# Optimization experiments

Hardware: AMD Instinct MI355X
Metric: run time of the kernel (lower is better)

Reference implementation:

```python
import jax, jax.numpy as jnp
import numpy as np
import math

HIDDEN = 1024
HEADS = 16
HEAD_DIM = HIDDEN // HEADS
B, S = 4, 2048


def setup_inputs() -> dict:
    key = jax.random.key(0)
    ks = jax.random.split(key, 10)
    scale = 1.0 / math.sqrt(HIDDEN)
    inp = {
        "x": jax.random.normal(ks[0], (B, S, HIDDEN), dtype=jnp.float32),
        "attention_mask": jnp.ones((B, 1, 1, S), dtype=jnp.int32),
        "Wq": jax.random.normal(ks[1], (HIDDEN, HIDDEN), dtype=jnp.float32) * scale,
        "bq": jnp.zeros((HIDDEN,), dtype=jnp.float32),
        "Wk": jax.random.normal(ks[2], (HIDDEN, HIDDEN), dtype=jnp.float32) * scale,
        "bk": jnp.zeros((HIDDEN,), dtype=jnp.float32),
        "Wv": jax.random.normal(ks[3], (HIDDEN, HIDDEN), dtype=jnp.float32) * scale,
        "bv": jnp.zeros((HIDDEN,), dtype=jnp.float32),
        "Wo": jax.random.normal(ks[4], (HIDDEN, HIDDEN), dtype=jnp.float32) * scale,
        "bo": jnp.zeros((HIDDEN,), dtype=jnp.float32),
    }
    return inp


def reference(x, attention_mask, Wq, bq, Wk, bk, Wv, bv, Wo, bo):
    b, s, d = x.shape
    # nn.Linear: x @ W.T + b
    q = (x @ Wq.T + bq).reshape(b, s, HEADS, HEAD_DIM).transpose(0, 2, 1, 3)
    k = (x @ Wk.T + bk).reshape(b, s, HEADS, HEAD_DIM).transpose(0, 2, 1, 3)
    v = (x @ Wv.T + bv).reshape(b, s, HEADS, HEAD_DIM).transpose(0, 2, 1, 3)
    # explicit O(S^2) score matrix, as in the original
    scores = jnp.einsum("bhqd,bhkd->bhqk", q, k) / math.sqrt(HEAD_DIM)
    scores = jnp.where(attention_mask == 0, jnp.float32(-1e9), scores)
    attn = jax.nn.softmax(scores, axis=-1)
    # dropout(p=0.1) treated as identity (eval mode) for a deterministic reference
    out = jnp.einsum("bhqk,bhkd->bhqd", attn, v)
    out = out.transpose(0, 2, 1, 3).reshape(b, s, d)
    return out @ Wo.T + bo
```

## Files before the change

### kernel.cpp

```cpp
#include <hip/hip_runtime.h>
#include <math.h>

#define HID 1024
#define NH  16
#define HD  64
#define NB  4
#define SL  2048
#define MROWS (NB * SL)

typedef __attribute__((ext_vector_type(8))) short short8;
typedef __attribute__((ext_vector_type(4))) float f32x4;
typedef unsigned short ushort_t;
typedef unsigned int uint_t;

__device__ __forceinline__ uint_t f2bf(float x) {
    union { float f; uint_t u; } a; a.f = x;
    return (a.u + 0x7fffu + ((a.u >> 16) & 1u)) >> 16;
}

__device__ __forceinline__ void load_lds16(const void* g, void* l) {
    __builtin_amdgcn_global_load_lds(
        (const __attribute__((address_space(1))) void*)g,
        (__attribute__((address_space(3))) void*)l, 16, 0, 0);
}

__device__ __forceinline__ void gemm_core_bk64(
    const ushort_t* __restrict__ A, const ushort_t* __restrict__ B,
    const int m0, const int n0, ushort_t* As, ushort_t* Bs, f32x4 (&acc)[4][4])
{
    const int tid = threadIdx.x;
    const int w = tid >> 6, lane = tid & 63;
    const int wm = (w & 1) << 6, wn = (w >> 1) << 6;
    const int c = lane & 15, quad = lane >> 4;

    for (int k0 = 0; k0 < HID; k0 += 64) {
        __syncthreads();
        #pragma unroll
        for (int rd = 0; rd < 4; ++rd) {
            const int g = rd * 4 + w;
            const int idx = g * 64 + lane;
            const int r = idx >> 3, sc = idx & 7;
            const int dc = sc ^ (r & 7);
            load_lds16(&A[(size_t)(m0 + r) * HID + k0 + dc * 8], As + g * 512);
            load_lds16(&B[(size_t)(n0 + r) * HID + k0 + dc * 8], Bs + g * 512);
        }
        __syncthreads();

        #pragma unroll
        for (int ks = 0; ks < 2; ++ks) {
            short8 af[4], bf[4];
            #pragma unroll
            for (int i = 0; i < 4; ++i) {
                const int ra = wm + i * 16 + c;
                const int rb = wn + i * 16 + c;
                af[i] = *(const short8*)
                    &As[ra * 64 + ((((ks << 2) + quad) ^ (c & 7)) << 3)];
                bf[i] = *(const short8*)
                    &Bs[rb * 64 + ((((ks << 2) + quad) ^ (c & 7)) << 3)];
            }
            #pragma unroll
            for (int i = 0; i < 4; ++i)
                #pragma unroll
                for (int j = 0; j < 4; ++j)
                    acc[i][j] = __builtin_amdgcn_mfma_f32_16x16x32_bf16(
                        af[i], bf[j], acc[i][j], 0, 0, 0);
        }
    }
}

__global__ __launch_bounds__(256) void cvt_bf16_kernel(
    const float* __restrict__ x,
    const float* __restrict__ wq, const float* __restrict__ wk,
    const float* __restrict__ wv, const float* __restrict__ wo,
    ushort_t* __restrict__ xb, ushort_t* __restrict__ wqb,
    ushort_t* __restrict__ wkb, ushort_t* __restrict__ wvb,
    ushort_t* __restrict__ wob)
{
    const int seg = blockIdx.y;
    const float* src; ushort_t* dst;
    if (seg < 8)       { src = x + (size_t)seg * 1048576; dst = xb + (size_t)seg * 1048576; }
    else if (seg == 8) { src = wq; dst = wqb; }
    else if (seg == 9) { src = wk; dst = wkb; }
    else if (seg == 10){ src = wv; dst = wvb; }
    else               { src = wo; dst = wob; }
    const int i = (blockIdx.x * 256 + threadIdx.x) * 8;
    const float4 a = *(const float4*)&src[i];
    const float4 b = *(const float4*)&src[i + 4];
    uint4 o;
    o.x = f2bf(a.x) | (f2bf(a.y) << 16);
    o.y = f2bf(a.z) | (f2bf(a.w) << 16);
    o.z = f2bf(b.x) | (f2bf(b.y) << 16);
    o.w = f2bf(b.z) | (f2bf(b.w) << 16);
    *(uint4*)&dst[i] = o;
}

__global__ __launch_bounds__(256) void qkv_mfma_kernel(
    const ushort_t* __restrict__ xb,
    const ushort_t* __restrict__ wqb, const ushort_t* __restrict__ wkb,
    const ushort_t* __restrict__ wvb,
    const float* __restrict__ bq, const float* __restrict__ bk,
    const float* __restrict__ bv,
    ushort_t* __restrict__ qo, ushort_t* __restrict__ ko,
    ushort_t* __restrict__ vo)
{
    __shared__ __align__(16) ushort_t As[128 * 64];
    __shared__ __align__(16) ushort_t Bs[128 * 64];

    const int wsel = blockIdx.z;
    const ushort_t* W    = (wsel == 0) ? wqb : (wsel == 1) ? wkb : wvb;
    const float*    bias = (wsel == 0) ? bq  : (wsel == 1) ? bk  : bv;
    const int m0 = blockIdx.y * 128, n0 = blockIdx.x * 128;

    f32x4 acc[4][4];
    const f32x4 zero = {0.f, 0.f, 0.f, 0.f};
    #pragma unroll
    for (int i = 0; i < 4; ++i)
        #pragma unroll
        for (int j = 0; j < 4; ++j) acc[i][j] = zero;

    gemm_core_bk64(xb, W, m0, n0, As, Bs, acc);

    const int tid = threadIdx.x;
    const int w = tid >> 6, lane = tid & 63;
    const int wm = (w & 1) << 6, wn = (w >> 1) << 6;
    const int c = lane & 15, quad = lane >> 4;
    const float qscale = (wsel == 0) ? 0.18033688f : 1.0f;

    #pragma unroll
    for (int j = 0; j < 4; ++j) {
        const int n_g = n0 + wn + j * 16 + c;
        const float bj = bias[n_g];
        const int h = n_g >> 6, d = n_g & 63;
        #pragma unroll
        for (int i = 0; i < 4; ++i) {
            const int mbase = m0 + wm + i * 16 + quad * 4;
            const int b = mbase >> 11;
            const int sbase = mbase & (SL - 1);
            if (wsel == 2) {
                ushort4 pk;
                pk.x = (ushort_t)f2bf(acc[i][j][0] + bj);
                pk.y = (ushort_t)f2bf(acc[i][j][1] + bj);
                pk.z = (ushort_t)f2bf(acc[i][j][2] + bj);
                pk.w = (ushort_t)f2bf(acc[i][j][3] + bj);
                *(ushort4*)&vo[(((size_t)(b * NH + h) * HD) + d) * SL + sbase] = pk;
            } else {
                ushort_t* dst = (wsel == 0) ? qo : ko;
                #pragma unroll
                for (int reg = 0; reg < 4; ++reg) {
                    const float v = (acc[i][j][reg] + bj) * qscale;
                    dst[(((size_t)(b * NH + h) * SL) + sbase + reg) * HD + d] =
                        (ushort_t)f2bf(v);
                }
            }
        }
    }
}

__global__ __launch_bounds__(256, 4) void attn_mfma_kernel(
    const ushort_t* __restrict__ q, const ushort_t* __restrict__ k,
    const ushort_t* __restrict__ vt, const int* __restrict__ mask,
    ushort_t* __restrict__ ao)
{
    __shared__ __align__(16) ushort_t Ks[64 * 64];
    __shared__ __align__(16) ushort_t Vs[64 * 64];
    __shared__ __align__(16) ushort_t Ps[128 * 64];

    const int qt = blockIdx.x;
    const int bh = blockIdx.y;
    const int b = bh >> 4, h = bh & 15;
    const int tid = threadIdx.x;
    const int w = tid >> 6, lane = tid & 63;
    const int c = lane & 15, quad = lane >> 4;

    const ushort_t* qp = q  + (size_t)bh * SL * HD + (size_t)qt * 128 * HD;
    const ushort_t* kp = k  + (size_t)bh * SL * HD;
    const ushort_t* vp = vt + (size_t)bh * HD * SL;

    short8 qf[2][2];
    #pragma unroll
    for (int mi = 0; mi < 2; ++mi)
        #pragma unroll
        for (int ks = 0; ks < 2; ++ks)
            qf[mi][ks] = *(const short8*)&qp[(size_t)(w * 32 + mi * 16 + c) * HD
                                             + ks * 32 + quad * 8];

    float l_s[2][4] = {};
    f32x4 oa[2][4];
    const f32x4 zero = {0.f, 0.f, 0.f, 0.f};
    #pragma unroll
    for (int mi = 0; mi < 2; ++mi)
        #pragma unroll
        for (int ni = 0; ni < 4; ++ni) oa[mi][ni] = zero;

    for (int kt = 0; kt < SL / 64; ++kt) {
        __syncthreads();
        #pragma unroll
        for (int rd = 0; rd < 2; ++rd) {
            const int g = rd * 4 + w;
            const int t = g * 64 + lane;
            const int r = t >> 3, sc = t & 7;
            const int dck = sc ^ ((r >> 2) & 7);
            const int dcv = sc ^ (r & 7);
            load_lds16(&kp[(size_t)(kt * 64 + r) * HD + dck * 8], Ks + g * 512);
            load_lds16(&vp[(size_t)r * SL + kt * 64 + dcv * 8], Vs + g * 512);
        }
        __syncthreads();

        f32x4 sf[2][4];
        #pragma unroll
        for (int mi = 0; mi < 2; ++mi)
            #pragma unroll
            for (int ni = 0; ni < 4; ++ni) sf[mi][ni] = zero;
        #pragma unroll
        for (int ni = 0; ni < 4; ++ni) {
            const int krow = 4 * c + ni;
            #pragma unroll
            for (int ks = 0; ks < 2; ++ks) {
                const short8 kf = *(const short8*)
                    &Ks[krow * 64 + (((ks * 4 + quad) ^ (c & 7)) << 3)];
                #pragma unroll
                for (int mi = 0; mi < 2; ++mi)
                    sf[mi][ni] = __builtin_amdgcn_mfma_f32_16x16x32_bf16(
                        qf[mi][ks], kf, sf[mi][ni], 0, 0, 0);
            }
        }

        const int4 mzv = *(const int4*)&mask[b * SL + kt * 64 + 4 * c];
        const int mz[4] = {mzv.x, mzv.y, mzv.z, mzv.w};

        #pragma unroll
        for (int mi = 0; mi < 2; ++mi) {
            #pragma unroll
            for (int reg = 0; reg < 4; ++reg) {
                float p[4];
                #pragma unroll
                for (int ni = 0; ni < 4; ++ni) {
                    float pv = __builtin_amdgcn_exp2f(sf[mi][ni][reg]);
                    p[ni] = (mz[ni] == 0) ? 0.f : pv;
                }
                l_s[mi][reg] += (p[0] + p[1]) + (p[2] + p[3]);
                union { float f; uint_t u; } u0, u1, u2, u3;
                u0.f = p[0]; u1.f = p[1]; u2.f = p[2]; u3.f = p[3];
                uint2 pk;
                pk.x = __builtin_amdgcn_perm(u1.u, u0.u, 0x07060302u);
                pk.y = __builtin_amdgcn_perm(u3.u, u2.u, 0x07060302u);
                const int prow = w * 32 + mi * 16 + quad * 4 + reg;
                *(uint2*)&Ps[prow * 64 + (((c >> 1) ^ (prow & 7)) * 8)
                             + ((c & 1) * 4)] = pk;
            }
        }

        short8 pf[2][2];
        #pragma unroll
        for (int mi = 0; mi < 2; ++mi)
            #pragma unroll
            for (int ks = 0; ks < 2; ++ks) {
                const int prow = w * 32 + mi * 16 + c;
                pf[mi][ks] = *(const short8*)
                    &Ps[prow * 64 + (((ks * 4 + quad) ^ (prow & 7)) << 3)];
            }
        #pragma unroll
        for (int ni = 0; ni < 4; ++ni) {
            const int n = ni * 16 + c;
            #pragma unroll
            for (int ks = 0; ks < 2; ++ks) {
                const short8 vf = *(const short8*)
                    &Vs[n * 64 + (((ks * 4 + quad) ^ (c & 7)) << 3)];
                #pragma unroll
                for (int mi = 0; mi < 2; ++mi)
                    oa[mi][ni] = __builtin_amdgcn_mfma_f32_16x16x32_bf16(
                        pf[mi][ks], vf, oa[mi][ni], 0, 0, 0);
            }
        }
    }

    #pragma unroll
    for (int mi = 0; mi < 2; ++mi) {
        #pragma unroll
        for (int reg = 0; reg < 4; ++reg) {
            float l = l_s[mi][reg];
            #pragma unroll
            for (int off = 1; off < 16; off <<= 1)
                l += __shfl_xor(l, off, 64);
            const float inv = 1.f / l;
            const int s_g = qt * 128 + w * 32 + mi * 16 + quad * 4 + reg;
            #pragma unroll
            for (int ni = 0; ni < 4; ++ni) {
                const int d = ni * 16 + c;
                ao[((size_t)(b * SL + s_g)) * HID + h * HD + d] =
                    (ushort_t)f2bf(oa[mi][ni][reg] * inv);
            }
        }
    }
}

__global__ __launch_bounds__(256) void out_mfma_kernel(
    const ushort_t* __restrict__ aob, const ushort_t* __restrict__ wob,
    const float* __restrict__ bo, float* __restrict__ out)
{
    __shared__ __align__(16) ushort_t As[128 * 64];
    __shared__ __align__(16) ushort_t Bs[128 * 64];

    const int m0 = blockIdx.y * 128, n0 = blockIdx.x * 128;

    f32x4 acc[4][4];
    const f32x4 zero = {0.f, 0.f, 0.f, 0.f};
    #pragma unroll
    for (int i = 0; i < 4; ++i)
        #pragma unroll
        for (int j = 0; j < 4; ++j) acc[i][j] = zero;

    gemm_core_bk64(aob, wob, m0, n0, As, Bs, acc);

    const int tid = threadIdx.x;
    const int w = tid >> 6, lane = tid & 63;
    const int wm = (w & 1) << 6, wn = (w >> 1) << 6;
    const int c = lane & 15, quad = lane >> 4;

    #pragma unroll
    for (int j = 0; j < 4; ++j) {
        const int n_g = n0 + wn + j * 16 + c;
        const float bj = bo[n_g];
        #pragma unroll
        for (int i = 0; i < 4; ++i) {
            const int mbase = m0 + wm + i * 16 + quad * 4;
            #pragma unroll
            for (int reg = 0; reg < 4; ++reg)
                out[(size_t)(mbase + reg) * HID + n_g] = acc[i][j][reg] + bj;
        }
    }
}

extern "C" void kernel_launch(void* const* d_in, const int* in_sizes, int n_in,
                              void* d_out, int out_size, void* d_ws, size_t ws_size,
                              hipStream_t stream)
{
    const float* x    = (const float*)d_in[0];
    const int*   mask = (const int*)d_in[1];
    const float* Wq   = (const float*)d_in[2];
    const float* bq   = (const float*)d_in[3];
    const float* Wk   = (const float*)d_in[4];
    const float* bk   = (const float*)d_in[5];
    const float* Wv   = (const float*)d_in[6];
    const float* bv   = (const float*)d_in[7];
    const float* Wo   = (const float*)d_in[8];
    const float* bo   = (const float*)d_in[9];
    float* out = (float*)d_out;

    ushort_t* p = (ushort_t*)d_ws;
    ushort_t* xb  = p; p += (size_t)MROWS * HID;
    ushort_t* wqb = p; p += (size_t)HID * HID;
    ushort_t* wkb = p; p += (size_t)HID * HID;
    ushort_t* wvb = p; p += (size_t)HID * HID;
    ushort_t* wob = p; p += (size_t)HID * HID;
    ushort_t* qb  = p; p += (size_t)MROWS * HID;
    ushort_t* kb  = p; p += (size_t)MROWS * HID;
    ushort_t* vtb = p; p += (size_t)MROWS * HID;
    ushort_t* aob = p; p += (size_t)MROWS * HID;

    cvt_bf16_kernel<<<dim3(512, 12), 256, 0, stream>>>(
        x, Wq, Wk, Wv, Wo, xb, wqb, wkb, wvb, wob);
    qkv_mfma_kernel<<<dim3(8, 64, 3), 256, 0, stream>>>(
        xb, wqb, wkb, wvb, bq, bk, bv, qb, kb, vtb);
    attn_mfma_kernel<<<dim3(16, 64), 256, 0, stream>>>(
        qb, kb, vtb, mask, aob);
    out_mfma_kernel<<<dim3(8, 64), 256, 0, stream>>>(
        aob, wob, bo, out);
}
```

Before: 296.0 us.

## Remap GEMM tiles per XCD and precompute attention LDS offsets

The QKV and output-projection GEMMs now remap the flat block index so that tiles sharing the same rows of the activation matrix land on the same XCD, aiming for better L2 reuse across the chiplets. Separately, the attention kernel hoists all swizzled LDS read and write offsets, the global K/V staging pointers and the mask pointer out of the key-tile loop, replacing per-iteration address arithmetic with pointer increments. The remapping assumes an 8x64 tile grid, and the hoisted offsets raise register pressure.

```diff
diff --git a/kernel.cpp b/kernel.cpp
--- a/kernel.cpp
+++ b/kernel.cpp
@@ -109,7 +109,11 @@
     const int wsel = blockIdx.z;
     const ushort_t* W    = (wsel == 0) ? wqb : (wsel == 1) ? wkb : wvb;
     const float*    bias = (wsel == 0) ? bq  : (wsel == 1) ? bk  : bv;
-    const int m0 = blockIdx.y * 128, n0 = blockIdx.x * 128;
+
+    const int flat = blockIdx.x + (blockIdx.y << 3);
+    const int xcd = flat & 7, s = flat >> 3;
+    const int m0 = ((xcd << 3) + (s >> 3)) * 128;
+    const int n0 = (s & 7) * 128;
 
     f32x4 acc[4][4];
     const f32x4 zero = {0.f, 0.f, 0.f, 0.f};
@@ -184,6 +188,39 @@
             qf[mi][ks] = *(const short8*)&qp[(size_t)(w * 32 + mi * 16 + c) * HD
                                              + ks * 32 + quad * 8];
 
+    int kfo[4][2], vfo[4][2], pfo[2][2], pwo[2][4];
+    #pragma unroll
+    for (int ni = 0; ni < 4; ++ni)
+        #pragma unroll
+        for (int ks = 0; ks < 2; ++ks) {
+            kfo[ni][ks] = (4 * c + ni) * 64 + (((ks * 4 + quad) ^ (c & 7)) << 3);
+            vfo[ni][ks] = (ni * 16 + c) * 64 + (((ks * 4 + quad) ^ (c & 7)) << 3);
+        }
+    #pragma unroll
+    for (int mi = 0; mi < 2; ++mi) {
+        #pragma unroll
+        for (int ks = 0; ks < 2; ++ks) {
+            const int prow = w * 32 + mi * 16 + c;
+            pfo[mi][ks] = prow * 64 + (((ks * 4 + quad) ^ (prow & 7)) << 3);
+        }
+        #pragma unroll
+        for (int reg = 0; reg < 4; ++reg) {
+            const int prow = w * 32 + mi * 16 + quad * 4 + reg;
+            pwo[mi][reg] = prow * 64 + (((c >> 1) ^ (prow & 7)) * 8)
+                           + ((c & 1) * 4);
+        }
+    }
+
+    const ushort_t* kst[2]; const ushort_t* vst[2];
+    #pragma unroll
+    for (int rd = 0; rd < 2; ++rd) {
+        const int t = (rd * 4 + w) * 64 + lane;
+        const int r = t >> 3, sc = t & 7;
+        kst[rd] = kp + (size_t)r * HD + (sc ^ ((r >> 2) & 7)) * 8;
+        vst[rd] = vp + (size_t)r * SL + (sc ^ (r & 7)) * 8;
+    }
+    const int* mp = mask + b * SL + 4 * c;
+
     float l_s[2][4] = {};
     f32x4 oa[2][4];
     const f32x4 zero = {0.f, 0.f, 0.f, 0.f};
@@ -194,16 +231,12 @@
 
     for (int kt = 0; kt < SL / 64; ++kt) {
         __syncthreads();
-        #pragma unroll
-        for (int rd = 0; rd < 2; ++rd) {
-            const int g = rd * 4 + w;
-            const int t = g * 64 + lane;
-            const int r = t >> 3, sc = t & 7;
-            const int dck = sc ^ ((r >> 2) & 7);
-            const int dcv = sc ^ (r & 7);
-            load_lds16(&kp[(size_t)(kt * 64 + r) * HD + dck * 8], Ks + g * 512);
-            load_lds16(&vp[(size_t)r * SL + kt * 64 + dcv * 8], Vs + g * 512);
-        }
+        load_lds16(kst[0], Ks + (0 * 4 + w) * 512);
+        load_lds16(vst[0], Vs + (0 * 4 + w) * 512);
+        load_lds16(kst[1], Ks + (1 * 4 + w) * 512);
+        load_lds16(vst[1], Vs + (1 * 4 + w) * 512);
+        kst[0] += 64 * HD; kst[1] += 64 * HD;
+        vst[0] += 64;      vst[1] += 64;
         __syncthreads();
 
         f32x4 sf[2][4];
@@ -213,11 +246,9 @@
             for (int ni = 0; ni < 4; ++ni) sf[mi][ni] = zero;
         #pragma unroll
         for (int ni = 0; ni < 4; ++ni) {
-            const int krow = 4 * c + ni;
             #pragma unroll
             for (int ks = 0; ks < 2; ++ks) {
-                const short8 kf = *(const short8*)
-                    &Ks[krow * 64 + (((ks * 4 + quad) ^ (c & 7)) << 3)];
+                const short8 kf = *(const short8*)&Ks[kfo[ni][ks]];
                 #pragma unroll
                 for (int mi = 0; mi < 2; ++mi)
                     sf[mi][ni] = __builtin_amdgcn_mfma_f32_16x16x32_bf16(
@@ -225,7 +256,8 @@
             }
         }
 
-        const int4 mzv = *(const int4*)&mask[b * SL + kt * 64 + 4 * c];
+        const int4 mzv = *(const int4*)mp;
+        mp += 64;
         const int mz[4] = {mzv.x, mzv.y, mzv.z, mzv.w};
 
         #pragma unroll
@@ -244,9 +276,7 @@
                 uint2 pk;
                 pk.x = __builtin_amdgcn_perm(u1.u, u0.u, 0x07060302u);
                 pk.y = __builtin_amdgcn_perm(u3.u, u2.u, 0x07060302u);
-                const int prow = w * 32 + mi * 16 + quad * 4 + reg;
-                *(uint2*)&Ps[prow * 64 + (((c >> 1) ^ (prow & 7)) * 8)
-                             + ((c & 1) * 4)] = pk;
+                *(uint2*)&Ps[pwo[mi][reg]] = pk;
             }
         }
 
@@ -254,18 +284,13 @@
         #pragma unroll
         for (int mi = 0; mi < 2; ++mi)
             #pragma unroll
+            for (int ks = 0; ks < 2; ++ks)
+                pf[mi][ks] = *(const short8*)&Ps[pfo[mi][ks]];
+        #pragma unroll
+        for (int ni = 0; ni < 4; ++ni) {
+            #pragma unroll
             for (int ks = 0; ks < 2; ++ks) {
-                const int prow = w * 32 + mi * 16 + c;
-                pf[mi][ks] = *(const short8*)
-                    &Ps[prow * 64 + (((ks * 4 + quad) ^ (prow & 7)) << 3)];
-            }
-        #pragma unroll
-        for (int ni = 0; ni < 4; ++ni) {
-            const int n = ni * 16 + c;
-            #pragma unroll
-            for (int ks = 0; ks < 2; ++ks) {
-                const short8 vf = *(const short8*)
-                    &Vs[n * 64 + (((ks * 4 + quad) ^ (c & 7)) << 3)];
+                const short8 vf = *(const short8*)&Vs[vfo[ni][ks]];
                 #pragma unroll
                 for (int mi = 0; mi < 2; ++mi)
                     oa[mi][ni] = __builtin_amdgcn_mfma_f32_16x16x32_bf16(
@@ -301,7 +326,10 @@
     __shared__ __align__(16) ushort_t As[128 * 64];
     __shared__ __align__(16) ushort_t Bs[128 * 64];
 
-    const int m0 = blockIdx.y * 128, n0 = blockIdx.x * 128;
+    const int flat = blockIdx.x + (blockIdx.y << 3);
+    const int xcd = flat & 7, s = flat >> 3;
+    const int m0 = ((xcd << 3) + (s >> 3)) * 128;
+    const int n0 = (s & 7) * 128;
 
     f32x4 acc[4][4];
     const f32x4 zero = {0.f, 0.f, 0.f, 0.f};
```

New measurement: 286.5 us. 3.2% less time.
